# Optimization experiments

Measured on AMD Instinct MI355X. Metric: run time of the kernel, lower is better.

The kernel has to match this reference:

```python
import jax, jax.numpy as jnp
import numpy as np

B, T, H, L, NH, FF, V, P = 8, 256, 768, 12, 12, 3072, 30522, 512
K, LH = 9, 256
DH = H // NH


def setup_inputs() -> dict:
    key = jax.random.key(0)
    kit = iter(jax.random.split(key, 48))
    rn = lambda shape: jax.random.normal(next(kit), shape, jnp.float32) * 0.02
    inp = {
        "input_ids": jax.random.randint(next(kit), (B, T), 0, V, dtype=jnp.int32),
        "attention_mask": jnp.ones((B, T), jnp.int32),
        "labels": jax.random.randint(next(kit), (B, T), 0, K, dtype=jnp.int32),
        "word_emb": rn((V, H)), "pos_emb": rn((P, H)), "type_emb": rn((2, H)),
        "emb_ln_g": jnp.ones((H,)), "emb_ln_b": jnp.zeros((H,)),
        "Wq": rn((L, H, H)), "bq": jnp.zeros((L, H)),
        "Wk": rn((L, H, H)), "bk": jnp.zeros((L, H)),
        "Wv": rn((L, H, H)), "bv": jnp.zeros((L, H)),
        "Wo": rn((L, H, H)), "bo": jnp.zeros((L, H)),
        "ln1_g": jnp.ones((L, H)), "ln1_b": jnp.zeros((L, H)),
        "Wf1": rn((L, H, FF)), "bf1": jnp.zeros((L, FF)),
        "Wf2": rn((L, FF, H)), "bf2": jnp.zeros((L, H)),
        "ln2_g": jnp.ones((L, H)), "ln2_b": jnp.zeros((L, H)),
        "w_ih_f": rn((4 * LH, H)), "w_hh_f": rn((4 * LH, LH)),
        "b_ih_f": jnp.zeros((4 * LH,)), "b_hh_f": jnp.zeros((4 * LH,)),
        "w_ih_b": rn((4 * LH, H)), "w_hh_b": rn((4 * LH, LH)),
        "b_ih_b": jnp.zeros((4 * LH,)), "b_hh_b": jnp.zeros((4 * LH,)),
        "W_clf": rn((2 * LH, K)), "b_clf": jnp.zeros((K,)),
        "crf_start": rn((K,)), "crf_end": rn((K,)), "crf_trans": rn((K, K)),
    }
    return inp


def _ln(x, g, b):
    m = jnp.mean(x, -1, keepdims=True)
    v = jnp.var(x, -1, keepdims=True)
    return (x - m) * jax.lax.rsqrt(v + 1e-12) * g + b


def _lstm(x, w_ih, w_hh, b_ih, b_hh, reverse):
    # PyTorch LSTM gate order: i, f, g, o. Precompute input gates: [T, B, 4*LH]
    xg = jnp.einsum('bth,gh->tbg', x, w_ih) + b_ih
    if reverse:
        xg = xg[::-1]

    def step(carry, g_in):
        h, c = carry
        g = g_in + h @ w_hh.T + b_hh
        i, f, gg, o = jnp.split(g, 4, axis=-1)
        c = jax.nn.sigmoid(f) * c + jax.nn.sigmoid(i) * jnp.tanh(gg)
        h = jax.nn.sigmoid(o) * jnp.tanh(c)
        return (h, c), h

    z = jnp.zeros((x.shape[0], w_hh.shape[1]), x.dtype)
    _, hs = jax.lax.scan(step, (z, z), xg)
    if reverse:
        hs = hs[::-1]
    return hs.transpose(1, 0, 2)  # [B, T, LH]


def reference(input_ids, attention_mask, labels, word_emb, pos_emb, type_emb,
              emb_ln_g, emb_ln_b, Wq, bq, Wk, bk, Wv, bv, Wo, bo, ln1_g, ln1_b,
              Wf1, bf1, Wf2, bf2, ln2_g, ln2_b, w_ih_f, w_hh_f, b_ih_f, b_hh_f,
              w_ih_b, w_hh_b, b_ih_b, b_hh_b, W_clf, b_clf,
              crf_start, crf_end, crf_trans):
    maskf = attention_mask.astype(jnp.float32)
    # ---- BERT embeddings ----
    x = word_emb[input_ids] + pos_emb[:T][None] + type_emb[0][None, None]
    x = _ln(x, emb_ln_g, emb_ln_b)
    attn_bias = (1.0 - maskf)[:, None, None, :] * -10000.0

    def layer(h, p):
        wq, bq_, wk, bk_, wv, bv_, wo, bo_, g1, b1, wf1, bf1_, wf2, bf2_, g2, b2 = p
        q = (h @ wq + bq_).reshape(B, T, NH, DH).transpose(0, 2, 1, 3)
        k = (h @ wk + bk_).reshape(B, T, NH, DH).transpose(0, 2, 1, 3)
        v = (h @ wv + bv_).reshape(B, T, NH, DH).transpose(0, 2, 1, 3)
        s = jnp.einsum('bhqd,bhkd->bhqk', q, k) * (1.0 / np.sqrt(DH)) + attn_bias
        ctx = jnp.einsum('bhqk,bhkd->bhqd', jax.nn.softmax(s, axis=-1), v)
        ctx = ctx.transpose(0, 2, 1, 3).reshape(B, T, H)
        a = _ln(h + ctx @ wo + bo_, g1, b1)
        f = jax.nn.gelu(a @ wf1 + bf1_, approximate=False) @ wf2 + bf2_
        return _ln(a + f, g2, b2), None

    x, _ = jax.lax.scan(layer, x, (Wq, bq, Wk, bk, Wv, bv, Wo, bo,
                                   ln1_g, ln1_b, Wf1, bf1, Wf2, bf2, ln2_g, ln2_b))

    # ---- BiLSTM + linear head -> emissions [B, T, K] ----
    hf = _lstm(x, w_ih_f, w_hh_f, b_ih_f, b_hh_f, False)
    hb = _lstm(x, w_ih_b, w_hh_b, b_ih_b, b_hh_b, True)
    em = jnp.concatenate([hf, hb], axis=-1) @ W_clf + b_clf

    # ---- CRF negative log-likelihood (torchcrf, reduction='mean'); model returns -llh ----
    # numerator: score of the gold path
    first = crf_start[labels[:, 0]] + jnp.take_along_axis(em[:, 0], labels[:, :1], 1)[:, 0]
    tr = crf_trans[labels[:, :-1], labels[:, 1:]]                      # [B, T-1]
    emt = jnp.take_along_axis(em[:, 1:], labels[:, 1:, None], 2)[..., 0]
    score = first + jnp.sum((tr + emt) * maskf[:, 1:], axis=1)
    ends = jnp.sum(maskf, axis=1).astype(jnp.int32) - 1
    last = jnp.take_along_axis(labels, ends[:, None], 1)[:, 0]
    score = score + crf_end[last]
    # denominator: log partition via forward algorithm
    alpha = crf_start[None] + em[:, 0]                                  # [B, K]

    def crf_step(alpha, inp):
        e_t, m_t = inp
        nxt = jax.nn.logsumexp(alpha[:, :, None] + crf_trans[None] + e_t[:, None, :], axis=1)
        return jnp.where(m_t[:, None] > 0, nxt, alpha), None

    alpha, _ = jax.lax.scan(crf_step, alpha,
                            (em[:, 1:].transpose(1, 0, 2), maskf[:, 1:].T))
    logZ = jax.nn.logsumexp(alpha + crf_end, axis=-1)
    return -jnp.mean(score - logZ)
```

## Files before the change

kernel.cpp:

```cpp
#include <hip/hip_runtime.h>
#include <math.h>

#define BB 8
#define TT 256
#define HH 768
#define NL 12
#define NH_ 12
#define DH_ 64
#define FF_ 3072
#define LH_ 256
#define KK_ 9

typedef unsigned char u8;
typedef unsigned short u16;
typedef unsigned int u32;
typedef __attribute__((ext_vector_type(4))) float f32x4;

static __device__ __forceinline__ float sigm_fast(float x) {
    return __builtin_amdgcn_rcpf(1.0f + __expf(-x));
}
static __device__ __forceinline__ float tanh_fast(float x) {
    return 1.0f - 2.0f * __builtin_amdgcn_rcpf(1.0f + __expf(2.0f * x));
}
static __device__ __forceinline__ float bf2f(u16 v) {
    return __uint_as_float(((u32)v) << 16);
}
static __device__ __forceinline__ u16 f2b16(float f) {
    u32 u = __float_as_uint(f);
    u += 0x7fffu + ((u >> 16) & 1u);
    return (u16)(u >> 16);
}
template <bool HI>
static __device__ __forceinline__ u32 pk8(float a, float b, u32 old) {
    return (u32)__builtin_amdgcn_cvt_pk_fp8_f32(a, b, (int)old, HI);
}
static __device__ __forceinline__ u8 f8(float v) {
    return (u8)(pk8<false>(v, v, 0) & 0xff);
}

static __device__ __forceinline__ f32x4 mfma_fp8(long a, long b, f32x4 c) {
    return __builtin_amdgcn_mfma_f32_16x16x32_fp8_fp8(a, b, c, 0, 0, 0);
}

#define GLL16(gp, lp) __builtin_amdgcn_global_load_lds( \
    (const __attribute__((address_space(1))) void*)(gp), \
    (__attribute__((address_space(3))) void*)(lp), 16, 0, 0)

static __device__ __forceinline__ float block_sum(float v, float* red) {
    int tid = threadIdx.x;
#pragma unroll
    for (int o = 32; o > 0; o >>= 1) v += __shfl_xor(v, o);
    if ((tid & 63) == 0) red[tid >> 6] = v;
    __syncthreads();
    return red[0] + red[1] + red[2] + red[3];
}

__global__ __launch_bounds__(256) void embed_ln_kernel(
    const int* __restrict__ ids, const float* __restrict__ we, const float* __restrict__ pe,
    const float* __restrict__ te, const float* __restrict__ g, const float* __restrict__ b,
    float* __restrict__ out, u8* __restrict__ out8) {
    int row = blockIdx.x;
    int t = row % TT;
    int id = ids[row];
    __shared__ float xr[HH];
    __shared__ float reda[8], redb[8];
    int tid = threadIdx.x;
    float s = 0.f;
    for (int h = tid; h < HH; h += 256) {
        float v = we[(size_t)id * HH + h] + pe[(size_t)t * HH + h] + te[h];
        xr[h] = v; s += v;
    }
    float mean = block_sum(s, reda) * (1.0f / HH);
    float vs = 0.f;
    for (int h = tid; h < HH; h += 256) { float d = xr[h] - mean; vs += d * d; }
    float var = block_sum(vs, redb) * (1.0f / HH);
    float rstd = rsqrtf(var + 1e-12f);
    for (int h = tid; h < HH; h += 256) {
        float v = (xr[h] - mean) * rstd * g[h] + b[h];
        out[(size_t)row * HH + h] = v;
        out8[(size_t)row * HH + h] = f8(v);
    }
}

__global__ __launch_bounds__(256) void ln_residual_kernel(
    const float* __restrict__ a, const float* __restrict__ f,
    const float* __restrict__ g, const float* __restrict__ b,
    float* __restrict__ out, u8* __restrict__ out8) {
    int row = blockIdx.x;
    __shared__ float xr[HH];
    __shared__ float reda[8], redb[8];
    int tid = threadIdx.x;
    float s = 0.f;
    for (int h = tid; h < HH; h += 256) {
        float v = a[(size_t)row * HH + h] + f[(size_t)row * HH + h];
        xr[h] = v; s += v;
    }
    float mean = block_sum(s, reda) * (1.0f / HH);
    float vs = 0.f;
    for (int h = tid; h < HH; h += 256) { float d = xr[h] - mean; vs += d * d; }
    float var = block_sum(vs, redb) * (1.0f / HH);
    float rstd = rsqrtf(var + 1e-12f);
    for (int h = tid; h < HH; h += 256) {
        float v = (xr[h] - mean) * rstd * g[h] + b[h];
        out[(size_t)row * HH + h] = v;
        out8[(size_t)row * HH + h] = f8(v);
    }
}

template <bool LAYERS12>
__global__ __launch_bounds__(256) void conv_w_kernel(
    const float* __restrict__ Wq, const float* __restrict__ Wk,
    const float* __restrict__ Wv, const float* __restrict__ Wo,
    const float* __restrict__ Wf1, const float* __restrict__ Wf2,
    u8* __restrict__ wbuf) {
    __shared__ float tile[64][65];
    int bid = blockIdx.x;
    int layer = 0;
    if (LAYERS12) { layer = bid / 1728; bid -= layer * 1728; }
    size_t woff = (size_t)layer * 7077888;
    size_t hh2 = (size_t)layer * HH * HH;
    size_t hf2 = (size_t)layer * HH * FF_;
    const float* src; u8* dst; int R, C, bx, by;
    if (bid < 576) {
        int m = bid / 144, t = bid % 144;
        src = (m == 0 ? Wq + hh2 : m == 1 ? Wk + hh2 : m == 2 ? Wv + hh2 : Wo + hh2);
        dst = wbuf + woff + (size_t)m * 589824;
        R = 768; C = 768; bx = t % 12; by = t / 12;
    } else if (bid < 1152) {
        int t = bid - 576;
        src = Wf1 + hf2; dst = wbuf + woff + 2359296; R = 768; C = 3072;
        bx = t % 48; by = t / 48;
    } else {
        int t = bid - 1152;
        src = Wf2 + hf2; dst = wbuf + woff + 4718592; R = 3072; C = 768;
        bx = t % 12; by = t / 12;
    }
    int tx = threadIdx.x & 15, ty = threadIdx.x >> 4;
#pragma unroll
    for (int p = 0; p < 4; ++p) {
        int row = p * 16 + ty;
        float4 v = *(const float4*)&src[(size_t)(by * 64 + row) * C + bx * 64 + tx * 4];
        tile[row][tx * 4 + 0] = v.x; tile[row][tx * 4 + 1] = v.y;
        tile[row][tx * 4 + 2] = v.z; tile[row][tx * 4 + 3] = v.w;
    }
    __syncthreads();
    int rq = (threadIdx.x & 15) * 4, cc0 = threadIdx.x >> 4;
#pragma unroll
    for (int p = 0; p < 4; ++p) {
        int cc = p * 16 + cc0;
        u32 w0 = pk8<false>(tile[rq][cc], tile[rq + 1][cc], 0);
        w0 = pk8<true>(tile[rq + 2][cc], tile[rq + 3][cc], w0);
        *(u32*)&dst[(size_t)(bx * 64 + cc) * R + by * 64 + rq] = w0;
    }
}

__global__ __launch_bounds__(256) void prep_kernel(
    const float* __restrict__ whf, const float* __restrict__ whb,
    const float* __restrict__ wif, const float* __restrict__ wib,
    u8* __restrict__ wfrag8, u8* __restrict__ wihT) {
    int bid = blockIdx.x;
    int tid = threadIdx.x;
    if (bid < 256) {
        int idx = bid * 256 + tid;
        int dir = idx >> 15;
        int kt  = (idx >> 12) & 7;
        int mt  = (idx >> 6) & 63;
        int lane = idx & 63;
        const float* W = dir ? whb : whf;
        int row = mt * 16 + (lane & 15);
        int k = kt * 32 + (lane >> 4) * 8;
        const float* src = W + (size_t)row * LH_ + k;
        u32 w0 = pk8<false>(src[0], src[1], 0);
        w0 = pk8<true>(src[2], src[3], w0);
        u32 w1 = pk8<false>(src[4], src[5], 0);
        w1 = pk8<true>(src[6], src[7], w1);
        uint2 pk; pk.x = w0; pk.y = w1;
        size_t base = (size_t)(((dir * 8 + kt) * 64 + mt) * 64 + lane) * 8;
        *(uint2*)&wfrag8[base] = pk;
    } else {
        int which = (bid < 1024) ? 0 : 1;
        const float* src = which ? wib : wif;
        u8* dst = wihT + (size_t)which * 786432;
        int i = (bid - (which ? 1024 : 256)) * 256 + tid;
        float4 v = *(const float4*)&src[(size_t)i * 4];
        u32 w0 = pk8<false>(v.x, v.y, 0);
        w0 = pk8<true>(v.z, v.w, w0);
        *(u32*)&dst[(size_t)i * 4] = w0;
    }
}

template <int BROWS>
__device__ __forceinline__ void stage8(
    const u8* __restrict__ S, int r0, int K, int k0, u8 (*lds)[128], int w, int lane) {
    int rsub = lane >> 3;
    int ap = lane & 7;
    constexpr int INSTS = BROWS / 32;
#pragma unroll
    for (int i = 0; i < INSTS; ++i) {
        int row0 = (w * INSTS + i) * 8;
        int row = row0 + rsub;
        int al = ap ^ (row & 7);
        GLL16(S + (size_t)(r0 + row) * K + k0 + al * 16, &lds[row0][0]);
    }
}

static __device__ __forceinline__ long lds8_read(const u8 (*lds)[128], int row, int g) {
    int a = g >> 1;
    int phys = a ^ (row & 7);
    return *(const long*)&lds[row][phys * 16 + (g & 1) * 8];
}

template <int BM, int BN, int OM, bool GELU, bool QKVW>
__global__ __launch_bounds__(256) void gemm3_kernel(
    const u8* __restrict__ A, const u8* __restrict__ BT,
    const float* __restrict__ b0, const float* __restrict__ b1, const float* __restrict__ b2,
    int seg, float* __restrict__ C, u8* __restrict__ C8, u16* __restrict__ C16,
    u8* __restrict__ vT, int M, int N, int K) {
    __shared__ u8 Als[2][BM][128];
    __shared__ u8 Bls[2][BN][128];
    int tid = threadIdx.x, lane = tid & 63, w = tid >> 6;
    int m0 = blockIdx.y * BM, n0 = blockIdx.x * BN;
    int wr = w >> 1, wc = w & 1;
    int l15 = lane & 15, q = lane >> 4;
    constexpr int MI = BM / 32;
    constexpr int NJ = BN / 32;

    f32x4 acc[MI][NJ];
#pragma unroll
    for (int mi = 0; mi < MI; ++mi)
#pragma unroll
        for (int nj = 0; nj < NJ; ++nj) acc[mi][nj] = (f32x4){0.f, 0.f, 0.f, 0.f};

    stage8<BM>(A, m0, K, 0, Als[0], w, lane);
    stage8<BN>(BT, n0, K, 0, Bls[0], w, lane);
    __syncthreads();
    int KT = K >> 7, cur = 0;
    for (int kt = 0; kt < KT; ++kt) {
        if (kt + 1 < KT) {
            stage8<BM>(A, m0, K, (kt + 1) << 7, Als[cur ^ 1], w, lane);
            stage8<BN>(BT, n0, K, (kt + 1) << 7, Bls[cur ^ 1], w, lane);
        }
#pragma unroll
        for (int ks = 0; ks < 4; ++ks) {
            int g = ks * 4 + q;
            long bfr[NJ];
#pragma unroll
            for (int nj = 0; nj < NJ; ++nj)
                bfr[nj] = lds8_read(Bls[cur], wc * (BN / 2) + nj * 16 + l15, g);
#pragma unroll
            for (int mi = 0; mi < MI; ++mi) {
                long a = lds8_read(Als[cur], wr * (BM / 2) + mi * 16 + l15, g);
#pragma unroll
                for (int nj = 0; nj < NJ; ++nj)
                    acc[mi][nj] = mfma_fp8(a, bfr[nj], acc[mi][nj]);
            }
        }
        __syncthreads();
        cur ^= 1;
    }

    int rbase = m0 + wr * (BM / 2) + q * 4;
    int cbase = n0 + wc * (BN / 2) + l15;
#pragma unroll
    for (int mi = 0; mi < MI; ++mi) {
#pragma unroll
        for (int nj = 0; nj < NJ; ++nj) {
            int col = cbase + nj * 16;
            int cc = col;
            const float* bp;
            if (cc < seg) bp = b0;
            else if (cc < 2 * seg) { bp = b1; cc -= seg; }
            else { bp = b2; cc -= 2 * seg; }
            float bias = bp[cc];
            if (QKVW && col >= 1536) {
                int hh = (col - 1536) >> 6, dl = (col - 1536) & 63;
                int brow = rbase + mi * 16;
                int bb = brow >> 8, t0 = brow & 255;
                u32 pkv = pk8<false>(acc[mi][nj][0] + bias, acc[mi][nj][1] + bias, 0);
                pkv = pk8<true>(acc[mi][nj][2] + bias, acc[mi][nj][3] + bias, pkv);
                *(u32*)&vT[(size_t)((bb * NH_ + hh) * DH_ + dl) * TT + t0] = pkv;
            } else {
#pragma unroll
                for (int j = 0; j < 4; ++j) {
                    int row = rbase + mi * 16 + j;
                    float v = acc[mi][nj][j] + bias;
                    if (GELU) v = 0.5f * v * (1.0f + erff(v * 0.70710678118654752f));
                    if (OM == 1) C8[(size_t)row * N + col] = f8(v);
                    else if (OM == 2) C16[(size_t)row * N + col] = f2b16(v);
                    else C[(size_t)row * N + col] = v;
                }
            }
        }
    }
}

__global__ __launch_bounds__(256) void attn_mfma_kernel(
    const u8* __restrict__ qkv8, const u8* __restrict__ vT,
    const int* __restrict__ mask, u8* __restrict__ ctx8) {
    int bid = blockIdx.x;
    int qb = bid & 3;
    int bh = bid >> 2;
    int b = bh / NH_, h = bh % NH_;
    int tid = threadIdx.x, lane = tid & 63, w = tid >> 6;
    int l15 = lane & 15, g4 = lane >> 4;
    __shared__ float bias_s[TT];
    __shared__ u8 P[64][260];
    for (int i = tid; i < TT; i += 256)
        bias_s[i] = (1.0f - (float)mask[b * TT + i]) * -10000.0f;
    __syncthreads();

    size_t qoff = (size_t)(b * TT + qb * 64 + w * 16 + l15) * 2304 + h * DH_ + g4 * 8;
    long aq0 = *(const long*)&qkv8[qoff];
    long aq1 = *(const long*)&qkv8[qoff + 32];

    f32x4 sacc[16];
#pragma unroll
    for (int nt = 0; nt < 16; ++nt) sacc[nt] = (f32x4){0.f, 0.f, 0.f, 0.f};
#pragma unroll
    for (int nt = 0; nt < 16; ++nt) {
        size_t koff = (size_t)(b * TT + nt * 16 + l15) * 2304 + 768 + h * DH_ + g4 * 8;
        long b0 = *(const long*)&qkv8[koff];
        long b1 = *(const long*)&qkv8[koff + 32];
        sacc[nt] = mfma_fp8(aq0, b0, sacc[nt]);
        sacc[nt] = mfma_fp8(aq1, b1, sacc[nt]);
    }
    float m[4] = {-1e30f, -1e30f, -1e30f, -1e30f};
#pragma unroll
    for (int nt = 0; nt < 16; ++nt) {
        float bv = bias_s[nt * 16 + l15];
#pragma unroll
        for (int j = 0; j < 4; ++j) {
            float s = sacc[nt][j] * 0.125f + bv;
            sacc[nt][j] = s;
            m[j] = fmaxf(m[j], s);
        }
    }
#pragma unroll
    for (int j = 0; j < 4; ++j) {
        m[j] = fmaxf(m[j], __shfl_xor(m[j], 1));
        m[j] = fmaxf(m[j], __shfl_xor(m[j], 2));
        m[j] = fmaxf(m[j], __shfl_xor(m[j], 4));
        m[j] = fmaxf(m[j], __shfl_xor(m[j], 8));
    }
    float l[4] = {0.f, 0.f, 0.f, 0.f};
#pragma unroll
    for (int nt = 0; nt < 16; ++nt) {
#pragma unroll
        for (int j = 0; j < 4; ++j) {
            float p = __expf(sacc[nt][j] - m[j]);
            sacc[nt][j] = p;
            l[j] += p;
        }
    }
#pragma unroll
    for (int j = 0; j < 4; ++j) {
        l[j] += __shfl_xor(l[j], 1);
        l[j] += __shfl_xor(l[j], 2);
        l[j] += __shfl_xor(l[j], 4);
        l[j] += __shfl_xor(l[j], 8);
    }
#pragma unroll
    for (int nt = 0; nt < 16; ++nt) {
#pragma unroll
        for (int j = 0; j < 4; ++j)
            P[w * 16 + g4 * 4 + j][nt * 16 + l15] = f8(sacc[nt][j]);
    }
    f32x4 oacc[4];
#pragma unroll
    for (int nt4 = 0; nt4 < 4; ++nt4) oacc[nt4] = (f32x4){0.f, 0.f, 0.f, 0.f};
    const u8* vbase = vT + (size_t)(bh * DH_) * TT;
#pragma unroll
    for (int ks = 0; ks < 8; ++ks) {
        long pa = *(const long*)&P[w * 16 + l15][ks * 32 + g4 * 8];
#pragma unroll
        for (int nt4 = 0; nt4 < 4; ++nt4) {
            long bv = *(const long*)&vbase[(size_t)(nt4 * 16 + l15) * TT + ks * 32 + g4 * 8];
            oacc[nt4] = mfma_fp8(pa, bv, oacc[nt4]);
        }
    }
    float inv[4];
#pragma unroll
    for (int j = 0; j < 4; ++j) inv[j] = __builtin_amdgcn_rcpf(l[j]);
    int rowg = b * TT + qb * 64 + w * 16 + g4 * 4;
#pragma unroll
    for (int nt4 = 0; nt4 < 4; ++nt4) {
        int col = h * DH_ + nt4 * 16 + l15;
#pragma unroll
        for (int j = 0; j < 4; ++j)
            ctx8[(size_t)(rowg + j) * HH + col] = f8(oacc[nt4][j] * inv[j]);
    }
}

__global__ __launch_bounds__(1024, 4) void lstm14_kernel(
    const u16* __restrict__ xgb, const u8* __restrict__ wfrag8,
    const float* __restrict__ bhh_f, const float* __restrict__ bhh_b,
    float* __restrict__ hf, float* __restrict__ hb) {
    int dir = blockIdx.x >> 3;
    int bat = blockIdx.x & 7;
    const u8* wf8 = wfrag8 + (size_t)dir * 262144;
    const float* bhh = dir ? bhh_b : bhh_f;
    float* hout = dir ? hb : hf;
    int tid = threadIdx.x, lane = tid & 63, wid = tid >> 6;
    __shared__ u8 wlds[4 * 64 * 512];
    __shared__ u8 h_f8[16][280];
    __shared__ u16 g_bf[1024][10];
    for (int i = tid; i < 16 * 280; i += 1024) ((u8*)h_f8)[i] = 0;
#pragma unroll
    for (int c = 0; c < 8; ++c) {
        int off = wid * 8192 + c * 1024;
        GLL16(wf8 + off + lane * 16, &wlds[off]);
    }
    long wst[4][4];
#pragma unroll
    for (int kt = 0; kt < 4; ++kt)
#pragma unroll
        for (int m = 0; m < 4; ++m) {
            wst[kt][m] = *(const long*)&wf8[(size_t)(((4 + kt) * 64) + wid * 4 + m) * 512 + lane * 8];
            asm volatile("" : "+v"(wst[kt][m]));
        }
    int l15 = lane & 15, qq = lane >> 4;
    int j = tid & 255;
    float bi_ = bhh[j], bf_ = bhh[256 + j], bg_ = bhh[512 + j], bo_ = bhh[768 + j];
    float c_r = 0.f;
    __syncthreads();
    for (int step = 0; step < TT; ++step) {
        int t = dir ? (TT - 1 - step) : step;
        float xgi = 0.f, xgf = 0.f, xgg = 0.f, xgo = 0.f;
        if (tid < 256) {
            size_t xa = ((size_t)(bat * TT + t)) * 2048 + (size_t)dir * 1024;
            xgi = bf2f(xgb[xa + j]);
            xgf = bf2f(xgb[xa + 256 + j]);
            xgg = bf2f(xgb[xa + 512 + j]);
            xgo = bf2f(xgb[xa + 768 + j]);
        }
        f32x4 acc[4];
#pragma unroll
        for (int m = 0; m < 4; ++m) acc[m] = (f32x4){0.f, 0.f, 0.f, 0.f};
#pragma unroll
        for (int kt = 0; kt < 4; ++kt) {
            long hfr = *(const long*)&h_f8[l15][kt * 32 + qq * 8];
#pragma unroll
            for (int m = 0; m < 4; ++m) {
                long a = *(const long*)&wlds[(size_t)(kt * 64 + wid * 4 + m) * 512 + lane * 8];
                acc[m] = mfma_fp8(a, hfr, acc[m]);
            }
        }
#pragma unroll
        for (int kt = 0; kt < 4; ++kt) {
            long hfr = *(const long*)&h_f8[l15][(4 + kt) * 32 + qq * 8];
#pragma unroll
            for (int m = 0; m < 4; ++m)
                acc[m] = mfma_fp8(wst[kt][m], hfr, acc[m]);
        }
        if (l15 == 0) {
#pragma unroll
            for (int m = 0; m < 4; ++m) {
                int R = (wid * 4 + m) * 16 + qq * 4;
#pragma unroll
                for (int jj = 0; jj < 4; ++jj)
                    g_bf[R + jj][0] = (u16)(__float_as_uint(acc[m][jj]) >> 16);
            }
        }
        __syncthreads();
        if (tid < 256) {
            float gi = xgi + bi_ + bf2f(g_bf[j][0]);
            float gf = xgf + bf_ + bf2f(g_bf[256 + j][0]);
            float gg = xgg + bg_ + bf2f(g_bf[512 + j][0]);
            float go = xgo + bo_ + bf2f(g_bf[768 + j][0]);
            float cc = sigm_fast(gf) * c_r + sigm_fast(gi) * tanh_fast(gg);
            c_r = cc;
            float hh = sigm_fast(go) * tanh_fast(cc);
            h_f8[0][j] = f8(hh);
            hout[((size_t)(bat * TT + t)) * LH_ + j] = hh;
        }
        __syncthreads();
    }
}

__global__ __launch_bounds__(256) void clf_kernel(
    const float* __restrict__ hf, const float* __restrict__ hb,
    const float* __restrict__ W, const float* __restrict__ bias, float* __restrict__ em) {
    int idx = blockIdx.x * blockDim.x + threadIdx.x;
    if (idx >= BB * TT * KK_) return;
    int row = idx / KK_, j = idx % KK_;
    float acc = bias[j];
    const float* hfp = hf + (size_t)row * LH_;
    const float* hbp = hb + (size_t)row * LH_;
    for (int kk = 0; kk < LH_; ++kk) acc += hfp[kk] * W[kk * KK_ + j];
    for (int kk = 0; kk < LH_; ++kk) acc += hbp[kk] * W[(LH_ + kk) * KK_ + j];
    em[idx] = acc;
}

__global__ __launch_bounds__(512) void crf2_kernel(
    const float* __restrict__ em, const int* __restrict__ labels, const int* __restrict__ mask,
    const float* __restrict__ cstart, const float* __restrict__ cend,
    const float* __restrict__ ctrans, float* __restrict__ out) {
    __shared__ float trans_s[81];
    __shared__ float res[8];
    int tid = threadIdx.x;
    int b = tid >> 6;
    int l = tid & 63;
    if (tid < 81) trans_s[tid] = ctrans[tid];
    __syncthreads();
    int lc = (l < 9) ? l : 0;
    float tcol[9];
#pragma unroll
    for (int i = 0; i < 9; ++i) tcol[i] = trans_s[i * 9 + lc];
    float alpha = (l < 9) ? cstart[lc] + em[(size_t)b * TT * KK_ + lc] : -1e30f;
    for (int t = 1; t < TT; ++t) {
        float e_t = (l < 9) ? em[((size_t)b * TT + t) * KK_ + lc] : 0.f;
        float m = -1e30f;
        float av[9];
#pragma unroll
        for (int i = 0; i < 9; ++i) {
            av[i] = __shfl(alpha, i) + tcol[i];
            m = fmaxf(m, av[i]);
        }
        float s = 0.f;
#pragma unroll
        for (int i = 0; i < 9; ++i) s += expf(av[i] - m);
        float nv = m + logf(s) + e_t;
        bool upd = (mask[b * TT + t] > 0) && (l < 9);
        alpha = upd ? nv : alpha;
    }
    float z = (l < 9) ? alpha + cend[lc] : -1e30f;
    float zm = z;
#pragma unroll
    for (int o = 32; o > 0; o >>= 1) zm = fmaxf(zm, __shfl_xor(zm, o));
    float zs = (l < 9) ? expf(z - zm) : 0.f;
#pragma unroll
    for (int o = 32; o > 0; o >>= 1) zs += __shfl_xor(zs, o);
    float logZ = zm + logf(zs);
    float sc = 0.f;
    int cnt = 0;
    for (int t = l; t < TT; t += 64) {
        cnt += mask[b * TT + t];
        if (t == 0) {
            int l0 = labels[b * TT];
            sc += cstart[l0] + em[(size_t)b * TT * KK_ + l0];
        } else {
            int lp = labels[b * TT + t - 1];
            int lt = labels[b * TT + t];
            sc += (trans_s[lp * KK_ + lt] + em[((size_t)b * TT + t) * KK_ + lt]) *
                  (float)mask[b * TT + t];
        }
    }
#pragma unroll
    for (int o = 32; o > 0; o >>= 1) { sc += __shfl_xor(sc, o); cnt += __shfl_xor(cnt, o); }
    if (l == 0) {
        int last = labels[b * TT + (cnt - 1)];
        sc += cend[last];
        res[b] = sc - logZ;
    }
    __syncthreads();
    if (tid == 0) {
        float acc = 0.f;
        for (int bb = 0; bb < BB; ++bb) acc += res[bb];
        out[0] = -acc / (float)BB;
    }
}

extern "C" void kernel_launch(void* const* d_in, const int* in_sizes, int n_in,
                              void* d_out, int out_size, void* d_ws, size_t ws_size,
                              hipStream_t stream) {
    const int* input_ids = (const int*)d_in[0];
    const int* attn_mask = (const int*)d_in[1];
    const int* labels    = (const int*)d_in[2];
    const float* word_emb = (const float*)d_in[3];
    const float* pos_emb  = (const float*)d_in[4];
    const float* type_emb = (const float*)d_in[5];
    const float* emb_ln_g = (const float*)d_in[6];
    const float* emb_ln_b = (const float*)d_in[7];
    const float* Wq = (const float*)d_in[8];
    const float* bq = (const float*)d_in[9];
    const float* Wk = (const float*)d_in[10];
    const float* bk = (const float*)d_in[11];
    const float* Wv = (const float*)d_in[12];
    const float* bv = (const float*)d_in[13];
    const float* Wo = (const float*)d_in[14];
    const float* bo = (const float*)d_in[15];
    const float* ln1_g = (const float*)d_in[16];
    const float* ln1_b = (const float*)d_in[17];
    const float* Wf1 = (const float*)d_in[18];
    const float* bf1 = (const float*)d_in[19];
    const float* Wf2 = (const float*)d_in[20];
    const float* bf2 = (const float*)d_in[21];
    const float* ln2_g = (const float*)d_in[22];
    const float* ln2_b = (const float*)d_in[23];
    const float* w_ih_f = (const float*)d_in[24];
    const float* w_hh_f = (const float*)d_in[25];
    const float* b_ih_f = (const float*)d_in[26];
    const float* b_hh_f = (const float*)d_in[27];
    const float* w_ih_b = (const float*)d_in[28];
    const float* w_hh_b = (const float*)d_in[29];
    const float* b_ih_b = (const float*)d_in[30];
    const float* b_hh_b = (const float*)d_in[31];
    const float* W_clf  = (const float*)d_in[32];
    const float* b_clf  = (const float*)d_in[33];
    const float* crf_start = (const float*)d_in[34];
    const float* crf_end   = (const float*)d_in[35];
    const float* crf_trans = (const float*)d_in[36];

    const size_t NTOK = (size_t)BB * TT;
    const size_t SZ = NTOK * HH;

    float* ws = (float*)d_ws;
    float* x    = ws;
    float* scr  = x + SZ;
    float* tmp  = scr + NTOK * 2304;
    float* ab   = tmp + SZ;
    u16* xg16   = (u16*)(ab + SZ);
    u8* x_f8    = (u8*)(xg16 + NTOK * 2048);
    u8* ab_f8   = x_f8 + SZ;
    u8* ctx_f8  = ab_f8 + SZ;
    u8* big_f8  = ctx_f8 + SZ;
    u8* qkv8    = big_f8 + NTOK * (size_t)FF_;
    u8* vT      = qkv8 + NTOK * 2304;
    u8* wihT    = vT + SZ;
    u8* wfrag8  = wihT + 1572864;
    u8* wbuf    = wfrag8 + 524288;
    const size_t base_off = (size_t)((u8*)wbuf - (u8*)d_ws);
    bool big = ws_size >= base_off + 12ull * 7077888ull + (1u << 20);

    float* hf = scr;
    float* hb = scr + 524288;
    float* em = scr + 1048576;

    embed_ln_kernel<<<NTOK, 256, 0, stream>>>(input_ids, word_emb, pos_emb, type_emb,
                                              emb_ln_g, emb_ln_b, x, x_f8);
    prep_kernel<<<1792, 256, 0, stream>>>(w_hh_f, w_hh_b, w_ih_f, w_ih_b, wfrag8, wihT);
    if (big)
        conv_w_kernel<true><<<1728 * 12, 256, 0, stream>>>(Wq, Wk, Wv, Wo, Wf1, Wf2, wbuf);

    dim3 gQKV(2304 / 128, NTOK / 128);
    dim3 gH(HH / 64, NTOK / 64);
    dim3 gF1(FF_ / 128, NTOK / 128);
    dim3 gG(2048 / 128, NTOK / 128);

    for (int l = 0; l < NL; ++l) {
        u8* wb = big ? wbuf + (size_t)l * 7077888 : wbuf;
        if (!big)
            conv_w_kernel<false><<<1728, 256, 0, stream>>>(
                Wq + (size_t)l * HH * HH, Wk + (size_t)l * HH * HH,
                Wv + (size_t)l * HH * HH, Wo + (size_t)l * HH * HH,
                Wf1 + (size_t)l * HH * FF_, Wf2 + (size_t)l * FF_ * HH, wb);

        const float* bq_l = bq + (size_t)l * HH;
        const float* bk_l = bk + (size_t)l * HH;
        const float* bv_l = bv + (size_t)l * HH;
        const float* bo_l = bo + (size_t)l * HH;
        const float* g1 = ln1_g + (size_t)l * HH;
        const float* b1 = ln1_b + (size_t)l * HH;
        const float* bf1_l = bf1 + (size_t)l * FF_;
        const float* bf2_l = bf2 + (size_t)l * HH;
        const float* g2 = ln2_g + (size_t)l * HH;
        const float* b2 = ln2_b + (size_t)l * HH;

        gemm3_kernel<128, 128, 1, false, true><<<gQKV, 256, 0, stream>>>(
            x_f8, wb, bq_l, bk_l, bv_l, 768, nullptr, qkv8, nullptr, vT, NTOK, 2304, HH);
        attn_mfma_kernel<<<BB * NH_ * 4, 256, 0, stream>>>(qkv8, vT, attn_mask, ctx_f8);
        gemm3_kernel<64, 64, 0, false, false><<<gH, 256, 0, stream>>>(
            ctx_f8, wb + 1769472, bo_l, bo_l, bo_l, 768, tmp, nullptr, nullptr, nullptr,
            NTOK, HH, HH);
        ln_residual_kernel<<<NTOK, 256, 0, stream>>>(x, tmp, g1, b1, ab, ab_f8);
        gemm3_kernel<128, 128, 1, true, false><<<gF1, 256, 0, stream>>>(
            ab_f8, wb + 2359296, bf1_l, bf1_l, bf1_l, FF_, nullptr, big_f8, nullptr, nullptr,
            NTOK, FF_, HH);
        gemm3_kernel<64, 64, 0, false, false><<<gH, 256, 0, stream>>>(
            big_f8, wb + 4718592, bf2_l, bf2_l, bf2_l, 768, tmp, nullptr, nullptr, nullptr,
            NTOK, HH, FF_);
        ln_residual_kernel<<<NTOK, 256, 0, stream>>>(ab, tmp, g2, b2, x, x_f8);
    }

    gemm3_kernel<128, 128, 2, false, false><<<gG, 256, 0, stream>>>(
        x_f8, wihT, b_ih_f, b_ih_b, b_ih_b, 1024, nullptr, nullptr, xg16, nullptr,
        NTOK, 2048, HH);

    lstm14_kernel<<<16, 1024, 0, stream>>>(xg16, wfrag8, b_hh_f, b_hh_b, hf, hb);
    clf_kernel<<<(BB * TT * KK_ + 255) / 256, 256, 0, stream>>>(hf, hb, W_clf, b_clf, em);
    crf2_kernel<<<1, 512, 0, stream>>>(em, labels, attn_mask, crf_start, crf_end, crf_trans,
                                       (float*)d_out);
}
```

Before: 1.978 ms.

## Remap LSTM gate tiles so each wave owns all four gates, removing one barrier

```diff
diff --git a/kernel.cpp b/kernel.cpp
--- a/kernel.cpp
+++ b/kernel.cpp
@@ -391,7 +391,7 @@
     }
 }
 
-__global__ __launch_bounds__(1024, 4) void lstm14_kernel(
+__global__ __launch_bounds__(1024, 4) void lstm16_kernel(
     const u16* __restrict__ xgb, const u8* __restrict__ wfrag8,
     const float* __restrict__ bhh_f, const float* __restrict__ bhh_b,
     float* __restrict__ hf, float* __restrict__ hb) {
@@ -400,14 +400,13 @@
     const u8* wf8 = wfrag8 + (size_t)dir * 262144;
     const float* bhh = dir ? bhh_b : bhh_f;
     float* hout = dir ? hb : hf;
-    int tid = threadIdx.x, lane = tid & 63, wid = tid >> 6;
+    int tid = threadIdx.x, lane = tid & 63, w = tid >> 6;
     __shared__ u8 wlds[4 * 64 * 512];
-    __shared__ u8 h_f8[16][280];
-    __shared__ u16 g_bf[1024][10];
-    for (int i = tid; i < 16 * 280; i += 1024) ((u8*)h_f8)[i] = 0;
+    __shared__ u8 h_f8[2][16][280];
+    for (int i = tid; i < 2 * 16 * 280; i += 1024) ((u8*)h_f8)[i] = 0;
 #pragma unroll
     for (int c = 0; c < 8; ++c) {
-        int off = wid * 8192 + c * 1024;
+        int off = w * 8192 + c * 1024;
         GLL16(wf8 + off + lane * 16, &wlds[off]);
     }
     long wst[4][4];
@@ -415,63 +414,79 @@
     for (int kt = 0; kt < 4; ++kt)
 #pragma unroll
         for (int m = 0; m < 4; ++m) {
-            wst[kt][m] = *(const long*)&wf8[(size_t)(((4 + kt) * 64) + wid * 4 + m) * 512 + lane * 8];
+            int mt = w + 16 * m;
+            wst[kt][m] = *(const long*)&wf8[(size_t)(((4 + kt) * 64 + mt) * 64 + lane) * 8];
             asm volatile("" : "+v"(wst[kt][m]));
         }
     int l15 = lane & 15, qq = lane >> 4;
-    int j = tid & 255;
-    float bi_ = bhh[j], bf_ = bhh[256 + j], bg_ = bhh[512 + j], bo_ = bhh[768 + j];
-    float c_r = 0.f;
+    bool upd = (l15 == 0);
+    int j0 = w * 16 + qq * 4;
+    float bi_[4], bf_[4], bg_[4], bo_[4], c_r[4];
+#pragma unroll
+    for (int jj = 0; jj < 4; ++jj) {
+        bi_[jj] = upd ? bhh[j0 + jj] : 0.f;
+        bf_[jj] = upd ? bhh[256 + j0 + jj] : 0.f;
+        bg_[jj] = upd ? bhh[512 + j0 + jj] : 0.f;
+        bo_[jj] = upd ? bhh[768 + j0 + jj] : 0.f;
+        c_r[jj] = 0.f;
+    }
     __syncthreads();
     for (int step = 0; step < TT; ++step) {
         int t = dir ? (TT - 1 - step) : step;
-        float xgi = 0.f, xgf = 0.f, xgg = 0.f, xgo = 0.f;
-        if (tid < 256) {
+        int cur = step & 1;
+        uint2 xi = {0, 0}, xf = {0, 0}, xg_ = {0, 0}, xo = {0, 0};
+        if (upd) {
             size_t xa = ((size_t)(bat * TT + t)) * 2048 + (size_t)dir * 1024;
-            xgi = bf2f(xgb[xa + j]);
-            xgf = bf2f(xgb[xa + 256 + j]);
-            xgg = bf2f(xgb[xa + 512 + j]);
-            xgo = bf2f(xgb[xa + 768 + j]);
+            xi = *(const uint2*)&xgb[xa + j0];
+            xf = *(const uint2*)&xgb[xa + 256 + j0];
+            xg_ = *(const uint2*)&xgb[xa + 512 + j0];
+            xo = *(const uint2*)&xgb[xa + 768 + j0];
         }
         f32x4 acc[4];
 #pragma unroll
         for (int m = 0; m < 4; ++m) acc[m] = (f32x4){0.f, 0.f, 0.f, 0.f};
 #pragma unroll
         for (int kt = 0; kt < 4; ++kt) {
-            long hfr = *(const long*)&h_f8[l15][kt * 32 + qq * 8];
+            long hfr = *(const long*)&h_f8[cur][l15][kt * 32 + qq * 8];
 #pragma unroll
             for (int m = 0; m < 4; ++m) {
-                long a = *(const long*)&wlds[(size_t)(kt * 64 + wid * 4 + m) * 512 + lane * 8];
+                int mt = w + 16 * m;
+                long a = *(const long*)&wlds[(size_t)(kt * 64 + mt) * 512 + lane * 8];
                 acc[m] = mfma_fp8(a, hfr, acc[m]);
             }
         }
 #pragma unroll
         for (int kt = 0; kt < 4; ++kt) {
-            long hfr = *(const long*)&h_f8[l15][(4 + kt) * 32 + qq * 8];
+            long hfr = *(const long*)&h_f8[cur][l15][(4 + kt) * 32 + qq * 8];
 #pragma unroll
             for (int m = 0; m < 4; ++m)
                 acc[m] = mfma_fp8(wst[kt][m], hfr, acc[m]);
         }
-        if (l15 == 0) {
-#pragma unroll
-            for (int m = 0; m < 4; ++m) {
-                int R = (wid * 4 + m) * 16 + qq * 4;
-#pragma unroll
-                for (int jj = 0; jj < 4; ++jj)
-                    g_bf[R + jj][0] = (u16)(__float_as_uint(acc[m][jj]) >> 16);
+        if (upd) {
+            float xiv[4] = { bf2f((u16)(xi.x & 0xffff)), bf2f((u16)(xi.x >> 16)),
+                             bf2f((u16)(xi.y & 0xffff)), bf2f((u16)(xi.y >> 16)) };
+            float xfv[4] = { bf2f((u16)(xf.x & 0xffff)), bf2f((u16)(xf.x >> 16)),
+                             bf2f((u16)(xf.y & 0xffff)), bf2f((u16)(xf.y >> 16)) };
+            float xgv[4] = { bf2f((u16)(xg_.x & 0xffff)), bf2f((u16)(xg_.x >> 16)),
+                             bf2f((u16)(xg_.y & 0xffff)), bf2f((u16)(xg_.y >> 16)) };
+            float xov[4] = { bf2f((u16)(xo.x & 0xffff)), bf2f((u16)(xo.x >> 16)),
+                             bf2f((u16)(xo.y & 0xffff)), bf2f((u16)(xo.y >> 16)) };
+            float hh[4];
+#pragma unroll
+            for (int jj = 0; jj < 4; ++jj) {
+                float gi = xiv[jj] + bi_[jj] + acc[0][jj];
+                float gf = xfv[jj] + bf_[jj] + acc[1][jj];
+                float gg = xgv[jj] + bg_[jj] + acc[2][jj];
+                float go = xov[jj] + bo_[jj] + acc[3][jj];
+                float cc = sigm_fast(gf) * c_r[jj] + sigm_fast(gi) * tanh_fast(gg);
+                c_r[jj] = cc;
+                hh[jj] = sigm_fast(go) * tanh_fast(cc);
             }
-        }
-        __syncthreads();
-        if (tid < 256) {
-            float gi = xgi + bi_ + bf2f(g_bf[j][0]);
-            float gf = xgf + bf_ + bf2f(g_bf[256 + j][0]);
-            float gg = xgg + bg_ + bf2f(g_bf[512 + j][0]);
-            float go = xgo + bo_ + bf2f(g_bf[768 + j][0]);
-            float cc = sigm_fast(gf) * c_r + sigm_fast(gi) * tanh_fast(gg);
-            c_r = cc;
-            float hh = sigm_fast(go) * tanh_fast(cc);
-            h_f8[0][j] = f8(hh);
-            hout[((size_t)(bat * TT + t)) * LH_ + j] = hh;
+            u32 pkh = pk8<false>(hh[0], hh[1], 0);
+            pkh = pk8<true>(hh[2], hh[3], pkh);
+            *(u32*)&h_f8[cur ^ 1][0][j0] = pkh;
+            float4 ho; ho.x = hh[0]; ho.y = hh[1]; ho.z = hh[2]; ho.w = hh[3];
+            *(float4*)&hout[((size_t)(bat * TT + t)) * LH_ + j0] = ho;
         }
         __syncthreads();
     }
@@ -507,8 +522,10 @@
 #pragma unroll
     for (int i = 0; i < 9; ++i) tcol[i] = trans_s[i * 9 + lc];
     float alpha = (l < 9) ? cstart[lc] + em[(size_t)b * TT * KK_ + lc] : -1e30f;
+    float e_next = (l < 9) ? em[((size_t)b * TT + 1) * KK_ + lc] : 0.f;
     for (int t = 1; t < TT; ++t) {
-        float e_t = (l < 9) ? em[((size_t)b * TT + t) * KK_ + lc] : 0.f;
+        float e_t = e_next;
+        if (t + 1 < TT) e_next = (l < 9) ? em[((size_t)b * TT + t + 1) * KK_ + lc] : 0.f;
         float m = -1e30f;
         float av[9];
 #pragma unroll
@@ -676,7 +693,7 @@
         x_f8, wihT, b_ih_f, b_ih_b, b_ih_b, 1024, nullptr, nullptr, xg16, nullptr,
         NTOK, 2048, HH);
 
-    lstm14_kernel<<<16, 1024, 0, stream>>>(xg16, wfrag8, b_hh_f, b_hh_b, hf, hb);
+    lstm16_kernel<<<16, 1024, 0, stream>>>(xg16, wfrag8, b_hh_f, b_hh_b, hf, hb);
     clf_kernel<<<(BB * TT * KK_ + 255) / 256, 256, 0, stream>>>(hf, hb, W_clf, b_clf, em);
     crf2_kernel<<<1, 512, 0, stream>>>(em, labels, attn_mask, crf_start, crf_end, crf_trans,
                                        (float*)d_out);
```

Measured after the change: 2.515 ms. +27.2%, slower.
